# Kernel tuning notes

Hardware: AMD Instinct MI355X
Metric: run time of the kernel (lower is better)

The kernel has to match this reference:

```python
import jax, jax.numpy as jnp
import numpy as np

NUM_HEADS = 12

def setup_inputs() -> dict:
    key = jax.random.key(0)
    k1, k2 = jax.random.split(key)
    X = jax.random.normal(k1, (2, 2048, 768), dtype=jnp.float32)
    # torch nn.Linear(dim, 2*dim, bias=False) weight has shape [2*dim, dim]
    W_qkv = jax.random.normal(k2, (1536, 768), dtype=jnp.float32) * (768 ** -0.5)
    return {"X": X, "W_qkv": W_qkv}

def reference(X, W_qkv):
    B, N, C = X.shape
    H = NUM_HEADS
    hd = C // H
    scale = hd ** -0.5
    # qkv: [B, N, 2, H, hd]
    qkv = (X @ W_qkv.T).reshape(B, N, 2, H, hd)
    q = jnp.transpose(qkv[:, :, 0], (0, 2, 1, 3))  # [B, H, N, hd]
    k = jnp.transpose(qkv[:, :, 1], (0, 2, 1, 3))  # [B, H, N, hd]
    attn = jnp.einsum('bhnd,bhmd->bhnm', q, k) * scale  # [B, H, N, N]
    # dropout p=0 -> identity; double sum over heads and keys
    scores = attn.sum(axis=1).sum(axis=-1)  # [B, N]
    return scores
```

## Files before the change

### kernel.cpp

```cpp
#include <hip/hip_runtime.h>


#define DIM 768
#define SEQ 2048
#define NGRP 16


__global__ void colsum_k(const float* __restrict__ X, float* __restrict__ xpart) {
    int bi = blockIdx.x;
    int b  = bi >> 8;
    int ch = bi & 255;
    int g  = ch >> 4;
    int i  = threadIdx.x;
    const float4* base = (const float4*)(X + ((size_t)b * SEQ + (size_t)ch * 8) * DIM) + i;
    float4 a = {0.f, 0.f, 0.f, 0.f};
    #pragma unroll
    for (int n = 0; n < 8; ++n) {
        float4 x = base[n * 192];
        a.x += x.x; a.y += x.y; a.z += x.z; a.w += x.w;
    }
    float* dst = xpart + ((size_t)(b * NGRP + g) * DIM) + i * 4;
    atomicAdd(dst + 0, a.x);
    atomicAdd(dst + 1, a.y);
    atomicAdd(dst + 2, a.z);
    atomicAdd(dst + 3, a.w);
}

__global__ void vt_k(const float* __restrict__ W, const float* __restrict__ xpart,
                     float* __restrict__ t) {
    __shared__ alignas(16) float xs[DIM];
    __shared__ float vv[64];
    int bi   = blockIdx.x;
    int b    = bi / 12;
    int c0   = (bi % 12) * 64;
    int tid  = threadIdx.x;
    int lane = tid & 63;
    int wv   = tid >> 6;

    #pragma unroll
    for (int k = 0; k < 3; ++k) {
        int d = tid + k * 256;
        const float* p = xpart + (size_t)(b * NGRP) * DIM + d;
        float s = 0.f;
        #pragma unroll
        for (int g = 0; g < NGRP; ++g)
            s += p[(size_t)g * DIM];
        xs[d] = s;
    }
    __syncthreads();

    {
        const float4* xs4 = (const float4*)xs;
        float4 s0 = xs4[lane];
        float4 s1 = xs4[lane + 64];
        float4 s2 = xs4[lane + 128];
        for (int i = 0; i < 16; ++i) {
            int j = wv * 16 + i;
            const float4* wr = (const float4*)(W + (size_t)(DIM + c0 + j) * DIM);
            float4 a0 = wr[lane];
            float4 a1 = wr[lane + 64];
            float4 a2 = wr[lane + 128];
            float acc = a0.x * s0.x + a0.y * s0.y + a0.z * s0.z + a0.w * s0.w
                      + a1.x * s1.x + a1.y * s1.y + a1.z * s1.z + a1.w * s1.w
                      + a2.x * s2.x + a2.y * s2.y + a2.z * s2.z + a2.w * s2.w;
            #pragma unroll
            for (int off = 32; off; off >>= 1) acc += __shfl_down(acc, off, 64);
            if (lane == 0) vv[j] = acc;
        }
    }
    __syncthreads();

    float* tb = t + b * DIM;
    #pragma unroll
    for (int k = 0; k < 3; ++k) {
        int d = tid + k * 256;
        const float* wq = W + (size_t)c0 * DIM + d;
        float acc = 0.f;
        #pragma unroll 8
        for (int j = 0; j < 64; ++j)
            acc += vv[j] * wq[(size_t)j * DIM];
        atomicAdd(&tb[d], acc);
    }
}

__global__ void scores_k(const float* __restrict__ X, const float* __restrict__ t,
                         float* __restrict__ out) {
    __shared__ alignas(16) float ft[DIM];
    int bi   = blockIdx.x;
    int b    = bi >> 8;
    int tid  = threadIdx.x;
    int lane = tid & 63;
    int wv   = tid >> 6;

    if (tid < 192)
        ((float4*)ft)[tid] = ((const float4*)(t + b * DIM))[tid];
    __syncthreads();

    const float4* t4 = (const float4*)ft;
    int r0 = bi * 8 + wv * 2;
    #pragma unroll
    for (int rr = 0; rr < 2; ++rr) {
        int r = r0 + rr;
        const float4* xr = (const float4*)(X + (size_t)r * DIM);
        float acc = 0.f;
        #pragma unroll
        for (int j = 0; j < 3; ++j) {
            float4 a = xr[lane + 64 * j];
            float4 s = t4[lane + 64 * j];
            acc += a.x * s.x + a.y * s.y + a.z * s.z + a.w * s.w;
        }
        #pragma unroll
        for (int off = 32; off; off >>= 1) acc += __shfl_down(acc, off, 64);
        if (lane == 0) out[r] = acc * 0.125f;
    }
}

extern "C" void kernel_launch(void* const* d_in, const int* in_sizes, int n_in,
                              void* d_out, int out_size, void* d_ws, size_t ws_size,
                              hipStream_t stream) {
    const float* X = (const float*)d_in[0];
    const float* W = (const float*)d_in[1];
    float* out = (float*)d_out;
    float* ws = (float*)d_ws;
    float* xpart = ws;
    float* t     = ws + 2 * NGRP * DIM;

    colsum_k<<<512, 192, 0, stream>>>(X, xpart);
    vt_k    <<<24, 256, 0, stream>>>(W, xpart, t);
    scores_k<<<512, 256, 0, stream>>>(X, t, out);
}
```

Before: 89.72 us.

## Split fused matvec kernel into two wide kernels to raise parallelism

```diff
diff --git a/kernel.cpp b/kernel.cpp
--- a/kernel.cpp
+++ b/kernel.cpp
@@ -19,20 +19,19 @@
         float4 x = base[n * 192];
         a.x += x.x; a.y += x.y; a.z += x.z; a.w += x.w;
     }
-    float* dst = xpart + ((size_t)(b * NGRP + g) * DIM) + i * 4;
+    float* dst = xpart + (size_t)(b * NGRP + g) * DIM + i * 4;
     atomicAdd(dst + 0, a.x);
     atomicAdd(dst + 1, a.y);
     atomicAdd(dst + 2, a.z);
     atomicAdd(dst + 3, a.w);
 }
 
-__global__ void vt_k(const float* __restrict__ W, const float* __restrict__ xpart,
-                     float* __restrict__ t) {
+__global__ void v_k(const float* __restrict__ W, const float* __restrict__ xpart,
+                    float* __restrict__ v) {
     __shared__ alignas(16) float xs[DIM];
-    __shared__ float vv[64];
     int bi   = blockIdx.x;
-    int b    = bi / 12;
-    int c0   = (bi % 12) * 64;
+    int b    = bi / 192;
+    int c0   = (bi % 192) * 4;
     int tid  = threadIdx.x;
     int lane = tid & 63;
     int wv   = tid >> 6;
@@ -49,38 +48,36 @@
     }
     __syncthreads();
 
-    {
-        const float4* xs4 = (const float4*)xs;
-        float4 s0 = xs4[lane];
-        float4 s1 = xs4[lane + 64];
-        float4 s2 = xs4[lane + 128];
-        for (int i = 0; i < 16; ++i) {
-            int j = wv * 16 + i;
-            const float4* wr = (const float4*)(W + (size_t)(DIM + c0 + j) * DIM);
-            float4 a0 = wr[lane];
-            float4 a1 = wr[lane + 64];
-            float4 a2 = wr[lane + 128];
-            float acc = a0.x * s0.x + a0.y * s0.y + a0.z * s0.z + a0.w * s0.w
-                      + a1.x * s1.x + a1.y * s1.y + a1.z * s1.z + a1.w * s1.w
-                      + a2.x * s2.x + a2.y * s2.y + a2.z * s2.z + a2.w * s2.w;
-            #pragma unroll
-            for (int off = 32; off; off >>= 1) acc += __shfl_down(acc, off, 64);
-            if (lane == 0) vv[j] = acc;
-        }
+    int c = c0 + wv;
+    const float4* wr  = (const float4*)(W + (size_t)(DIM + c) * DIM);
+    const float4* xs4 = (const float4*)xs;
+    float acc = 0.f;
+    #pragma unroll
+    for (int j = 0; j < 3; ++j) {
+        float4 a = wr[lane + 64 * j];
+        float4 s = xs4[lane + 64 * j];
+        acc += a.x * s.x + a.y * s.y + a.z * s.z + a.w * s.w;
     }
-    __syncthreads();
+    #pragma unroll
+    for (int off = 32; off; off >>= 1) acc += __shfl_down(acc, off, 64);
+    if (lane == 0) v[b * DIM + c] = acc;
+}
 
-    float* tb = t + b * DIM;
-    #pragma unroll
-    for (int k = 0; k < 3; ++k) {
-        int d = tid + k * 256;
-        const float* wq = W + (size_t)c0 * DIM + d;
-        float acc = 0.f;
-        #pragma unroll 8
-        for (int j = 0; j < 64; ++j)
-            acc += vv[j] * wq[(size_t)j * DIM];
-        atomicAdd(&tb[d], acc);
-    }
+__global__ void t_k(const float* __restrict__ W, const float* __restrict__ v,
+                    float* __restrict__ t) {
+    int bi  = blockIdx.x;
+    int b   = bi / 96;
+    int rem = bi % 96;
+    int cs  = rem / 3;
+    int dch = rem % 3;
+    int d   = dch * 256 + threadIdx.x;
+    int c0  = cs * 24;
+    const float* vb = v + b * DIM;
+    float acc = 0.f;
+    #pragma unroll 8
+    for (int c = c0; c < c0 + 24; ++c)
+        acc += W[(size_t)c * DIM + d] * vb[c];
+    atomicAdd(&t[b * DIM + d], acc);
 }
 
 __global__ void scores_k(const float* __restrict__ X, const float* __restrict__ t,
@@ -123,9 +120,11 @@
     float* out = (float*)d_out;
     float* ws = (float*)d_ws;
     float* xpart = ws;
-    float* t     = ws + 2 * NGRP * DIM;
+    float* v     = ws + 2 * NGRP * DIM;
+    float* t     = v + 2 * DIM;
 
     colsum_k<<<512, 192, 0, stream>>>(X, xpart);
-    vt_k    <<<24, 256, 0, stream>>>(W, xpart, t);
+    v_k     <<<384, 256, 0, stream>>>(W, xpart, v);
+    t_k     <<<192, 256, 0, stream>>>(W, v, t);
     scores_k<<<512, 256, 0, stream>>>(X, t, out);
 }
```

Result: faster. 76.79 us (-14.4%).
